# Performance work log

Hardware: AMD Instinct MI355X
Metric: run time of the kernel (lower is better)

The kernel has to match this reference:

```python
import jax, jax.numpy as jnp
import numpy as np
import math

B, T, D, H = 4, 1024, 1024, 16
DK = D // H
TAU_THRESH = 0.3


def setup_inputs() -> dict:
    key = jax.random.key(0)
    ks = jax.random.split(key, 13)
    s = 1.0 / math.sqrt(D)
    return {
        "x": jax.random.normal(ks[0], (B, T, D), dtype=jnp.float32),
        "Wq": jax.random.normal(ks[1], (D, D), dtype=jnp.float32) * s,
        "bq": jax.random.normal(ks[2], (D,), dtype=jnp.float32) * s,
        "Wk": jax.random.normal(ks[3], (D, D), dtype=jnp.float32) * s,
        "bk": jax.random.normal(ks[4], (D,), dtype=jnp.float32) * s,
        "Wv": jax.random.normal(ks[5], (D, D), dtype=jnp.float32) * s,
        "bv": jax.random.normal(ks[6], (D,), dtype=jnp.float32) * s,
        "Wo": jax.random.normal(ks[7], (D, D), dtype=jnp.float32) * s,
        "bo": jax.random.normal(ks[8], (D,), dtype=jnp.float32) * s,
        "Wg1": jax.random.normal(ks[9], (1, D), dtype=jnp.float32) * s,
        "bg1": jax.random.normal(ks[10], (1,), dtype=jnp.float32) * s,
        "Wg2": jax.random.normal(ks[11], (1, D), dtype=jnp.float32) * s,
        "bg2": jax.random.normal(ks[12], (1,), dtype=jnp.float32) * s,
    }


def reference(x, Wq, bq, Wk, bk, Wv, bv, Wo, bo, Wg1, bg1, Wg2, bg2):
    b, t, d = x.shape
    # projections (torch Linear: y = x @ W.T + b)
    Q = (x @ Wq.T + bq).reshape(b, t, H, DK).transpose(0, 2, 1, 3)  # [B,H,T,dk]
    K = (x @ Wk.T + bk).reshape(b, t, H, DK).transpose(0, 2, 1, 3)
    V = (x @ Wv.T + bv).reshape(b, t, H, DK).transpose(0, 2, 1, 3)
    scores = jnp.einsum("bhqd,bhkd->bhqk", Q, K) / math.sqrt(DK)  # [B,H,T,T]
    # confidence gates from first-token query context [B, H*dk] = [B, D]
    context = Q[:, :, 0, :].reshape(b, d)
    q1 = jax.nn.sigmoid(context @ Wg1.T + bg1)  # [B,1]
    q2 = jax.nn.sigmoid(context @ Wg2.T + bg2)  # [B,1]
    c = jnp.clip(q1 * q2, 1e-8, 1.0)            # [B,1]
    tau = jnp.where(c < TAU_THRESH, 1.0 / c, jnp.ones_like(c)).reshape(b, 1, 1, 1)
    p = jax.nn.softmax(scores / tau, axis=-1)
    cb = c.reshape(b, 1, 1, 1)
    p_gated = cb * p + (1.0 - cb) * (1.0 / t)
    u = jnp.mean(1.0 - c, axis=-1, keepdims=True)  # [B,1]
    attn_out = jnp.einsum("bhqk,bhkd->bhqd", p_gated, V)
    attn_out = attn_out.transpose(0, 2, 1, 3).reshape(b, t, d)
    output = attn_out @ Wo.T + bo
    return output, u
```

## Files before the change

### kernel.cpp

```cpp
#include <hip/hip_runtime.h>
#include <stdint.h>

typedef short bf16x8 __attribute__((ext_vector_type(8)));
typedef float f32x4 __attribute__((ext_vector_type(4)));

#define MFMA_BF16(a, b, c) __builtin_amdgcn_mfma_f32_16x16x32_bf16((a), (b), (c), 0, 0, 0)

__device__ __forceinline__ short f2bf(float x) {
  union { float f; uint32_t u; } v; v.f = x;
  uint32_t r = (v.u + 0x7FFFu + ((v.u >> 16) & 1u)) >> 16;
  return (short)r;
}
__device__ __forceinline__ uint32_t rnd_bf_hi(float x) {
  union { float f; uint32_t u; } v; v.f = x;
  return v.u + 0x7FFFu + ((v.u >> 16) & 1u);
}
__device__ __forceinline__ uint32_t pack2bf(float a, float b) {
  return __builtin_amdgcn_perm(rnd_bf_hi(b), rnd_bf_hi(a), 0x07060302);
}
__device__ __forceinline__ float bfbits2f(uint32_t b16) {
  union { uint32_t u; float f; } v; v.u = b16 << 16; return v.f;
}
__device__ __forceinline__ float fexp2(float x) {
#if __has_builtin(__builtin_amdgcn_exp2f)
  return __builtin_amdgcn_exp2f(x);
#else
  return __expf(x * 0.6931471805599453f);
#endif
}
__device__ __forceinline__ void async16(const void* g, void* l) {
  __builtin_amdgcn_global_load_lds(
      (const __attribute__((address_space(1))) uint32_t*)g,
      (__attribute__((address_space(3))) uint32_t*)l, 16, 0, 0);
}

__global__ __launch_bounds__(256) void prep_k(
    const float* __restrict__ x, const float* __restrict__ Wq,
    const float* __restrict__ Wk, const float* __restrict__ Wv,
    const float* __restrict__ Wo, const float* __restrict__ bq,
    short* __restrict__ xb, short* __restrict__ Wqb, short* __restrict__ Wkb,
    short* __restrict__ Wvb, short* __restrict__ Wob, float* __restrict__ ctx) {
  __shared__ float xs[1024];
  const int bid = blockIdx.x;
  const int tid = threadIdx.x;
  if (bid < 8192) {
    const float* src; short* dst; int idx;
    if (bid < 4096) {
      src = x; dst = xb; idx = (bid << 8) + tid;
    } else {
      const int r = bid - 4096;
      const int z = r >> 10;
      src = (z == 0) ? Wq : (z == 1) ? Wk : (z == 2) ? Wv : Wo;
      dst = (z == 0) ? Wqb : (z == 1) ? Wkb : (z == 2) ? Wvb : Wob;
      idx = ((r & 1023) << 8) + tid;
    }
    float4 v = ((const float4*)src)[idx];
    short4 o;
    o.x = f2bf(v.x); o.y = f2bf(v.y); o.z = f2bf(v.z); o.w = f2bf(v.w);
    ((short4*)dst)[idx] = o;
  } else {
    const int r = bid - 8192;
    const int b = r >> 4;
    const int n0 = (r & 15) << 6;
    for (int i = tid; i < 1024; i += 256) xs[i] = x[b * 1048576 + i];
    __syncthreads();
    const int w = tid >> 6, lane = tid & 63;
    const float4* xv4 = (const float4*)xs;
    for (int rr = 0; rr < 16; ++rr) {
      const int n = n0 + (w << 4) + rr;
      const float4* wrow = (const float4*)(Wq + n * 1024);
      float p = 0.f;
#pragma unroll
      for (int c2 = 0; c2 < 4; ++c2) {
        float4 wv = wrow[lane + (c2 << 6)];
        float4 xv = xv4[lane + (c2 << 6)];
        p += xv.x * wv.x + xv.y * wv.y + xv.z * wv.z + xv.w * wv.w;
      }
#pragma unroll
      for (int off = 32; off; off >>= 1) p += __shfl_xor(p, off);
      if (lane == 0) ctx[b * 1024 + n] = p + bq[n];
    }
  }
}

__global__ __launch_bounds__(256) void gates_fin(const float* __restrict__ ctx,
                                                 const float* __restrict__ Wg1,
                                                 const float* __restrict__ bg1,
                                                 const float* __restrict__ Wg2,
                                                 const float* __restrict__ bg2,
                                                 float* __restrict__ gates,
                                                 float* __restrict__ u_out) {
  __shared__ float red[16];
  const int tid = threadIdx.x, w = tid >> 6, lane = tid & 63;
  for (int b = 0; b < 4; ++b) {
    float4 cv = ((const float4*)(ctx + b * 1024))[tid];
    float4 w1 = ((const float4*)Wg1)[tid];
    float4 w2 = ((const float4*)Wg2)[tid];
    float p1 = cv.x * w1.x + cv.y * w1.y + cv.z * w1.z + cv.w * w1.w;
    float p2 = cv.x * w2.x + cv.y * w2.y + cv.z * w2.z + cv.w * w2.w;
#pragma unroll
    for (int off = 32; off; off >>= 1) { p1 += __shfl_xor(p1, off); p2 += __shfl_xor(p2, off); }
    if (lane == 0) { red[w] = p1; red[8 + w] = p2; }
    __syncthreads();
    if (tid == 0) {
      float g1 = red[0] + red[1] + red[2] + red[3] + bg1[0];
      float g2 = red[8] + red[9] + red[10] + red[11] + bg2[0];
      float q1 = 1.f / (1.f + expf(-g1));
      float q2 = 1.f / (1.f + expf(-g2));
      float c = fminf(fmaxf(q1 * q2, 1e-8f), 1.0f);
      gates[b * 2 + 0] = c;
      gates[b * 2 + 1] = (c < 0.3f ? c : 1.0f) * 0.125f;
      u_out[b] = 1.0f - c;
    }
    __syncthreads();
  }
}

__global__ __launch_bounds__(256) void gemm_qkv(
    const short* __restrict__ xb,
    const short* __restrict__ Wqb, const short* __restrict__ Wkb, const short* __restrict__ Wvb,
    const float* __restrict__ bq, const float* __restrict__ bk, const float* __restrict__ bv,
    const float* __restrict__ gat,
    short* __restrict__ Qh, short* __restrict__ Kh, short* __restrict__ Vt) {
  const int z = blockIdx.z;
  const short* W = (z == 0) ? Wqb : (z == 1) ? Wkb : Wvb;
  const float* bias = (z == 0) ? bq : (z == 1) ? bk : bv;

  const int m0 = blockIdx.x << 7;
  const int n0 = blockIdx.y << 7;
  const int tid = threadIdx.x;
  const int w = tid >> 6, lane = tid & 63;
  const int m15 = lane & 15, quad = lane >> 4;
  const int wr = w >> 1, wc = w & 1;

  const float qsc = (z == 0) ? gat[(m0 >> 10) * 2 + 1] * 1.4426950408889634f : 1.0f;

  __shared__ short As[4096];
  __shared__ short Bs[4096];

  f32x4 acc[4][4];
#pragma unroll
  for (int i = 0; i < 4; ++i)
#pragma unroll
    for (int j = 0; j < 4; ++j) { f32x4 zz = {0.f, 0.f, 0.f, 0.f}; acc[i][j] = zz; }

  const int s0 = tid, s1 = tid + 256;
  const int row0 = s0 >> 2, lcb0 = (s0 & 3) ^ ((row0 >> 1) & 3);
  const int row1 = s1 >> 2, lcb1 = (s1 & 3) ^ ((row1 >> 1) & 3);
  const short* ga0 = xb + (m0 + row0) * 1024 + (lcb0 << 3);
  const short* ga1 = xb + (m0 + row1) * 1024 + (lcb1 << 3);
  const short* gb0 = W + (n0 + row0) * 1024 + (lcb0 << 3);
  const short* gb1 = W + (n0 + row1) * 1024 + (lcb1 << 3);
  short* la0 = &As[s0 << 3];
  short* la1 = &As[s1 << 3];
  short* lb0 = &Bs[s0 << 3];
  short* lb1 = &Bs[s1 << 3];

  for (int kt = 0; kt < 32; ++kt) {
    async16(ga0, la0); async16(ga1, la1);
    async16(gb0, lb0); async16(gb1, lb1);
    ga0 += 32; ga1 += 32; gb0 += 32; gb1 += 32;
    __syncthreads();
    bf16x8 a[4], b[4];
#pragma unroll
    for (int i = 0; i < 4; ++i) {
      const int ra = (wr << 6) + (i << 4) + m15;
      a[i] = *(const bf16x8*)(&As[ra * 32 + ((quad ^ ((ra >> 1) & 3)) << 3)]);
    }
#pragma unroll
    for (int j = 0; j < 4; ++j) {
      const int rb = (wc << 6) + (j << 4) + m15;
      b[j] = *(const bf16x8*)(&Bs[rb * 32 + ((quad ^ ((rb >> 1) & 3)) << 3)]);
    }
#pragma unroll
    for (int i = 0; i < 4; ++i)
#pragma unroll
      for (int j = 0; j < 4; ++j)
        acc[i][j] = MFMA_BF16(a[i], b[j], acc[i][j]);
    __syncthreads();
  }

  if (z == 2) {
    const int batch = m0 >> 10;
#pragma unroll
    for (int j = 0; j < 4; ++j) {
      const int n = n0 + (wc << 6) + (j << 4) + m15;
      const float bb_ = bias[n];
      const int h = n >> 6, dk = n & 63;
      short* vrow = Vt + ((((batch << 4) + h) << 6) + dk) * 1024;
#pragma unroll
      for (int i = 0; i < 4; ++i) {
        const int t = (m0 & 1023) + (wr << 6) + (i << 4) + (quad << 2);
        uint2 pk;
        pk.x = pack2bf(acc[i][j][0] + bb_, acc[i][j][1] + bb_);
        pk.y = pack2bf(acc[i][j][2] + bb_, acc[i][j][3] + bb_);
        *(uint2*)(vrow + t) = pk;
      }
    }
  } else {
#pragma unroll
    for (int j = 0; j < 4; ++j) {
      const int n = n0 + (wc << 6) + (j << 4) + m15;
      const float bb_ = bias[n];
      const int h = n >> 6, dk = n & 63;
#pragma unroll
      for (int i = 0; i < 4; ++i) {
        const int mb = m0 + (wr << 6) + (i << 4) + (quad << 2);
#pragma unroll
        for (int r = 0; r < 4; ++r) {
          const int m = mb + r;
          const int batch = m >> 10, t = m & 1023;
          const short o = f2bf((acc[i][j][r] + bb_) * qsc);
          if (z == 1) Kh[((batch * 16 + h) * 1024 + t) * 64 + dk] = o;
          else        Qh[((batch * 16 + h) * 1024 + t) * 64 + dk] = o;
        }
      }
    }
  }
}

__global__ __launch_bounds__(256) void gemm_out(const short* __restrict__ Ab,
                                                const short* __restrict__ Wo,
                                                const float* __restrict__ bo,
                                                float* __restrict__ Cout) {
  const int m0 = blockIdx.x << 6;
  const int n0 = blockIdx.y << 7;
  const int tid = threadIdx.x;
  const int w = tid >> 6, lane = tid & 63;
  const int m15 = lane & 15, quad = lane >> 4;
  const int wr = w >> 1, wc = w & 1;

  __shared__ short As[2048];
  __shared__ short Bs[4096];

  f32x4 acc[2][4];
#pragma unroll
  for (int i = 0; i < 2; ++i)
#pragma unroll
    for (int j = 0; j < 4; ++j) { f32x4 zz = {0.f, 0.f, 0.f, 0.f}; acc[i][j] = zz; }

  const int s0 = tid, s1 = tid + 256;
  const int arow = s0 >> 2, alcb = (s0 & 3) ^ ((arow >> 1) & 3);
  const int brow0 = s0 >> 2, blcb0 = alcb;
  const int brow1 = s1 >> 2, blcb1 = (s1 & 3) ^ ((brow1 >> 1) & 3);
  const short* gA  = Ab + (m0 + arow) * 1024 + (alcb << 3);
  const short* gB0 = Wo + (n0 + brow0) * 1024 + (blcb0 << 3);
  const short* gB1 = Wo + (n0 + brow1) * 1024 + (blcb1 << 3);
  short* lA  = &As[s0 << 3];
  short* lB0 = &Bs[s0 << 3];
  short* lB1 = &Bs[s1 << 3];

  for (int kt = 0; kt < 32; ++kt) {
    async16(gA, lA);
    async16(gB0, lB0); async16(gB1, lB1);
    gA += 32; gB0 += 32; gB1 += 32;
    __syncthreads();
    bf16x8 a[2], b[4];
#pragma unroll
    for (int i = 0; i < 2; ++i) {
      const int ra = (wr << 5) + (i << 4) + m15;
      a[i] = *(const bf16x8*)(&As[ra * 32 + ((quad ^ ((ra >> 1) & 3)) << 3)]);
    }
#pragma unroll
    for (int j = 0; j < 4; ++j) {
      const int rb = (wc << 6) + (j << 4) + m15;
      b[j] = *(const bf16x8*)(&Bs[rb * 32 + ((quad ^ ((rb >> 1) & 3)) << 3)]);
    }
#pragma unroll
    for (int i = 0; i < 2; ++i)
#pragma unroll
      for (int j = 0; j < 4; ++j)
        acc[i][j] = MFMA_BF16(a[i], b[j], acc[i][j]);
    __syncthreads();
  }

#pragma unroll
  for (int j = 0; j < 4; ++j) {
    const int n = n0 + (wc << 6) + (j << 4) + m15;
    const float bb_ = bo[n];
#pragma unroll
    for (int i = 0; i < 2; ++i) {
      const int mb = m0 + (wr << 5) + (i << 4) + (quad << 2);
#pragma unroll
      for (int r = 0; r < 4; ++r)
        Cout[(mb + r) * 1024 + n] = acc[i][j][r] + bb_;
    }
  }
}

__global__ __launch_bounds__(256) void meanv_k(const short* __restrict__ Vt,
                                               float* __restrict__ meanV) {
  const int bh = blockIdx.x;
  const int tid = threadIdx.x;
  const int d = tid >> 2, part = tid & 3;
  const short* row = Vt + bh * 65536 + d * 1024 + part * 256;
  float s = 0.f;
#pragma unroll 4
  for (int i = 0; i < 64; ++i) {
    uint2 v = *(const uint2*)(row + i * 4);
    s += bfbits2f(v.x & 0xffffu) + bfbits2f(v.x >> 16) +
         bfbits2f(v.y & 0xffffu) + bfbits2f(v.y >> 16);
  }
  s += __shfl_xor(s, 1);
  s += __shfl_xor(s, 2);
  if (part == 0) meanV[bh * 64 + d] = s * (1.0f / 1024.0f);
}

__global__ __launch_bounds__(256, 4) void attn_k(const short* __restrict__ Qh,
                                                 const short* __restrict__ Kh,
                                                 const short* __restrict__ Vt,
                                                 const float* __restrict__ gates,
                                                 const float* __restrict__ meanV,
                                                 short* __restrict__ attnb) {
  const int bh = blockIdx.x;
  const int b = bh >> 4, h = bh & 15;
  const int q0 = blockIdx.y << 6;
  const int tid = threadIdx.x;
  const int w = tid >> 6, lane = tid & 63;
  const int m15 = lane & 15, quad = lane >> 4;

  __shared__ short Ks[2][4096];
  __shared__ short Vs[2][4096];

  const short* ksrc = Kh + bh * 65536;
  const short* vsrc = Vt + bh * 65536;

  const short* qsrc = Qh + ((bh << 10) + q0 + (w << 4) + m15) * 64;
  const bf16x8 qb0 = *(const bf16x8*)(qsrc + (quad << 3));
  const bf16x8 qb1 = *(const bf16x8*)(qsrc + 32 + (quad << 3));

  const int off0 = tid, off1 = tid + 256;
  const int r0 = off0 >> 3, cb0 = (off0 & 7) ^ (r0 & 7);
  const int r1 = off1 >> 3, cb1 = (off1 & 7) ^ (r1 & 7);

#define STAGE(kv, bufi)                                                        \
  do {                                                                         \
    async16(ksrc + (((kv) << 6) + r0) * 64 + (cb0 << 3), &Ks[bufi][off0 << 3]);\
    async16(ksrc + (((kv) << 6) + r1) * 64 + (cb1 << 3), &Ks[bufi][off1 << 3]);\
    async16(vsrc + r0 * 1024 + ((kv) << 6) + (cb0 << 3), &Vs[bufi][off0 << 3]);\
    async16(vsrc + r1 * 1024 + ((kv) << 6) + (cb1 << 3), &Vs[bufi][off1 << 3]);\
  } while (0)

  STAGE(0, 0);

  float lsum = 0.f;
  f32x4 o_acc[4];
#pragma unroll
  for (int jd = 0; jd < 4; ++jd) { f32x4 zz = {0.f, 0.f, 0.f, 0.f}; o_acc[jd] = zz; }

  const int srcA = ((quad & 1) << 5) + m15;
  const int srcB = srcA + 16;
  const bool selhi = (quad & 2) != 0;

  for (int kv = 0; kv < 16; ++kv) {
    __syncthreads();
    if (kv < 15) STAGE(kv + 1, (kv + 1) & 1);
    const short* Kb = &Ks[kv & 1][0];
    const short* Vb = &Vs[kv & 1][0];

    f32x4 sacc[4];
#pragma unroll
    for (int s = 0; s < 4; ++s) {
      const int row = (s << 4) + m15;
      const int sw = row & 7;
      bf16x8 a0 = *(const bf16x8*)(Kb + (row << 6) + ((quad ^ sw) << 3));
      bf16x8 a1 = *(const bf16x8*)(Kb + (row << 6) + (((quad + 4) ^ sw) << 3));
      f32x4 zz = {0.f, 0.f, 0.f, 0.f};
      zz = MFMA_BF16(a0, qb0, zz);
      zz = MFMA_BF16(a1, qb1, zz);
      sacc[s] = zz;
    }

    uint32_t pk[4][2];
#pragma unroll
    for (int s = 0; s < 4; ++s) {
      float p0 = fexp2(sacc[s][0]);
      float p1 = fexp2(sacc[s][1]);
      float p2 = fexp2(sacc[s][2]);
      float p3 = fexp2(sacc[s][3]);
      lsum += (p0 + p1) + (p2 + p3);
      pk[s][0] = pack2bf(p0, p1);
      pk[s][1] = pack2bf(p2, p3);
    }

    bf16x8 pf[2];
#pragma unroll
    for (int H = 0; H < 2; ++H) {
      uint32_t f[4];
#pragma unroll
      for (int rp = 0; rp < 2; ++rp) {
        uint32_t alo = (uint32_t)__shfl((int)pk[2 * H][rp], srcA);
        uint32_t ahi = (uint32_t)__shfl((int)pk[2 * H + 1][rp], srcA);
        uint32_t blo = (uint32_t)__shfl((int)pk[2 * H][rp], srcB);
        uint32_t bhi = (uint32_t)__shfl((int)pk[2 * H + 1][rp], srcB);
        f[rp]     = selhi ? ahi : alo;
        f[2 + rp] = selhi ? bhi : blo;
      }
      pf[H] = *(bf16x8*)f;
    }

#pragma unroll
    for (int jd = 0; jd < 4; ++jd) {
      const int row = (jd << 4) + m15;
      const int sw = row & 7;
      bf16x8 v0 = *(const bf16x8*)(Vb + (row << 6) + ((quad ^ sw) << 3));
      bf16x8 v1 = *(const bf16x8*)(Vb + (row << 6) + (((quad + 4) ^ sw) << 3));
      o_acc[jd] = MFMA_BF16(v0, pf[0], o_acc[jd]);
      o_acc[jd] = MFMA_BF16(v1, pf[1], o_acc[jd]);
    }
  }
#undef STAGE

  float l = lsum;
  l += __shfl_xor(l, 16);
  l += __shfl_xor(l, 32);

  const float cg = gates[b * 2 + 0];
  const float s0 = cg / l;
  const float omc = 1.0f - cg;
  const int qrow = q0 + (w << 4) + m15;
  short* orow = attnb + ((b << 10) + qrow) * 1024 + (h << 6);
#pragma unroll
  for (int jd = 0; jd < 4; ++jd) {
    float4 mv = *(const float4*)(meanV + (bh << 6) + (jd << 4) + (quad << 2));
    float v0_ = s0 * o_acc[jd][0] + omc * mv.x;
    float v1_ = s0 * o_acc[jd][1] + omc * mv.y;
    float v2_ = s0 * o_acc[jd][2] + omc * mv.z;
    float v3_ = s0 * o_acc[jd][3] + omc * mv.w;
    uint2 st;
    st.x = pack2bf(v0_, v1_);
    st.y = pack2bf(v2_, v3_);
    *(uint2*)(orow + (jd << 4) + (quad << 2)) = st;
  }
}

extern "C" void kernel_launch(void* const* d_in, const int* in_sizes, int n_in,
                              void* d_out, int out_size, void* d_ws, size_t ws_size,
                              hipStream_t stream) {
  const float* x   = (const float*)d_in[0];
  const float* Wq  = (const float*)d_in[1];
  const float* bq  = (const float*)d_in[2];
  const float* Wk  = (const float*)d_in[3];
  const float* bk  = (const float*)d_in[4];
  const float* Wv  = (const float*)d_in[5];
  const float* bv  = (const float*)d_in[6];
  const float* Wo  = (const float*)d_in[7];
  const float* bo  = (const float*)d_in[8];
  const float* Wg1 = (const float*)d_in[9];
  const float* bg1 = (const float*)d_in[10];
  const float* Wg2 = (const float*)d_in[11];
  const float* bg2 = (const float*)d_in[12];
  float* out = (float*)d_out;

  char* ws = (char*)d_ws;
  short* xb   = (short*)(ws + 0);
  short* Wqb  = (short*)(ws + 8388608);
  short* Wkb  = (short*)(ws + 10485760);
  short* Wvb  = (short*)(ws + 12582912);
  short* Wob  = (short*)(ws + 14680064);
  short* Qh   = (short*)(ws + 16777216);
  short* Kh   = (short*)(ws + 25165824);
  short* Vt   = (short*)(ws + 33554432);
  short* attb = (short*)(ws + 41943040);
  float* ctx  = (float*)(ws + 50331648);
  float* gat  = (float*)(ws + 50348032);
  float* mV   = (float*)(ws + 50348064);

  prep_k<<<8256, 256, 0, stream>>>(x, Wq, Wk, Wv, Wo, bq,
                                   xb, Wqb, Wkb, Wvb, Wob, ctx);
  gates_fin<<<1, 256, 0, stream>>>(ctx, Wg1, bg1, Wg2, bg2, gat, out + 4194304);

  gemm_qkv<<<dim3(32, 8, 3), 256, 0, stream>>>(xb, Wqb, Wkb, Wvb, bq, bk, bv, gat, Qh, Kh, Vt);
  meanv_k<<<64, 256, 0, stream>>>(Vt, mV);
  attn_k<<<dim3(64, 16), 256, 0, stream>>>(Qh, Kh, Vt, gat, mV, attb);
  gemm_out<<<dim3(64, 8), 256, 0, stream>>>(attb, Wob, bo, out);
}
```

Measured before the change: 218.6 us.

## Move softmax scale into attention, drop LDS swizzle and packed Vt stores

The temperature/log2e scale moves from Q at projection time into the attention exp (multiply per score). The QKV GEMM drops the XOR LDS swizzle in favour of a plain row layout, and replaces the packed 8-byte transposed V stores with per-element scalar stores. The mean-of-V division by 1024 moves into the attention epilogue coefficient. These changes add a per-score multiply, likely LDS bank conflicts, and uncoalesced V writes, so they read more like a simplification than a speedup.

```diff
diff --git a/kernel.cpp b/kernel.cpp
--- a/kernel.cpp
+++ b/kernel.cpp
@@ -109,7 +109,7 @@
       float q2 = 1.f / (1.f + expf(-g2));
       float c = fminf(fmaxf(q1 * q2, 1e-8f), 1.0f);
       gates[b * 2 + 0] = c;
-      gates[b * 2 + 1] = (c < 0.3f ? c : 1.0f) * 0.125f;
+      gates[b * 2 + 1] = (c < 0.3f ? c : 1.0f) * 0.125f * 1.4426950408889634f;
       u_out[b] = 1.0f - c;
     }
     __syncthreads();
@@ -120,7 +120,6 @@
     const short* __restrict__ xb,
     const short* __restrict__ Wqb, const short* __restrict__ Wkb, const short* __restrict__ Wvb,
     const float* __restrict__ bq, const float* __restrict__ bk, const float* __restrict__ bv,
-    const float* __restrict__ gat,
     short* __restrict__ Qh, short* __restrict__ Kh, short* __restrict__ Vt) {
   const int z = blockIdx.z;
   const short* W = (z == 0) ? Wqb : (z == 1) ? Wkb : Wvb;
@@ -133,8 +132,6 @@
   const int m15 = lane & 15, quad = lane >> 4;
   const int wr = w >> 1, wc = w & 1;
 
-  const float qsc = (z == 0) ? gat[(m0 >> 10) * 2 + 1] * 1.4426950408889634f : 1.0f;
-
   __shared__ short As[4096];
   __shared__ short Bs[4096];
 
@@ -144,17 +141,16 @@
 #pragma unroll
     for (int j = 0; j < 4; ++j) { f32x4 zz = {0.f, 0.f, 0.f, 0.f}; acc[i][j] = zz; }
 
-  const int s0 = tid, s1 = tid + 256;
-  const int row0 = s0 >> 2, lcb0 = (s0 & 3) ^ ((row0 >> 1) & 3);
-  const int row1 = s1 >> 2, lcb1 = (s1 & 3) ^ ((row1 >> 1) & 3);
-  const short* ga0 = xb + (m0 + row0) * 1024 + (lcb0 << 3);
-  const short* ga1 = xb + (m0 + row1) * 1024 + (lcb1 << 3);
-  const short* gb0 = W + (n0 + row0) * 1024 + (lcb0 << 3);
-  const short* gb1 = W + (n0 + row1) * 1024 + (lcb1 << 3);
-  short* la0 = &As[s0 << 3];
-  short* la1 = &As[s1 << 3];
-  short* lb0 = &Bs[s0 << 3];
-  short* lb1 = &Bs[s1 << 3];
+  const int srow = (w << 5) + (lane >> 2);
+  const int scol = (lane & 3) << 3;
+  const short* ga0 = xb + (m0 + srow) * 1024 + scol;
+  const short* ga1 = ga0 + 16 * 1024;
+  const short* gb0 = W + (n0 + srow) * 1024 + scol;
+  const short* gb1 = gb0 + 16 * 1024;
+  short* la0 = &As[srow * 32 + scol];
+  short* la1 = la0 + 512;
+  short* lb0 = &Bs[srow * 32 + scol];
+  short* lb1 = lb0 + 512;
 
   for (int kt = 0; kt < 32; ++kt) {
     async16(ga0, la0); async16(ga1, la1);
@@ -163,15 +159,11 @@
     __syncthreads();
     bf16x8 a[4], b[4];
 #pragma unroll
-    for (int i = 0; i < 4; ++i) {
-      const int ra = (wr << 6) + (i << 4) + m15;
-      a[i] = *(const bf16x8*)(&As[ra * 32 + ((quad ^ ((ra >> 1) & 3)) << 3)]);
-    }
-#pragma unroll
-    for (int j = 0; j < 4; ++j) {
-      const int rb = (wc << 6) + (j << 4) + m15;
-      b[j] = *(const bf16x8*)(&Bs[rb * 32 + ((quad ^ ((rb >> 1) & 3)) << 3)]);
-    }
+    for (int i = 0; i < 4; ++i)
+      a[i] = *(const bf16x8*)(&As[((wr << 6) + (i << 4) + m15) * 32 + (quad << 3)]);
+#pragma unroll
+    for (int j = 0; j < 4; ++j)
+      b[j] = *(const bf16x8*)(&Bs[((wc << 6) + (j << 4) + m15) * 32 + (quad << 3)]);
 #pragma unroll
     for (int i = 0; i < 4; ++i)
 #pragma unroll
@@ -180,39 +172,25 @@
     __syncthreads();
   }
 
-  if (z == 2) {
-    const int batch = m0 >> 10;
-#pragma unroll
-    for (int j = 0; j < 4; ++j) {
-      const int n = n0 + (wc << 6) + (j << 4) + m15;
-      const float bb_ = bias[n];
-      const int h = n >> 6, dk = n & 63;
-      short* vrow = Vt + ((((batch << 4) + h) << 6) + dk) * 1024;
-#pragma unroll
-      for (int i = 0; i < 4; ++i) {
-        const int t = (m0 & 1023) + (wr << 6) + (i << 4) + (quad << 2);
-        uint2 pk;
-        pk.x = pack2bf(acc[i][j][0] + bb_, acc[i][j][1] + bb_);
-        pk.y = pack2bf(acc[i][j][2] + bb_, acc[i][j][3] + bb_);
-        *(uint2*)(vrow + t) = pk;
-      }
-    }
-  } else {
-#pragma unroll
-    for (int j = 0; j < 4; ++j) {
-      const int n = n0 + (wc << 6) + (j << 4) + m15;
-      const float bb_ = bias[n];
-      const int h = n >> 6, dk = n & 63;
-#pragma unroll
-      for (int i = 0; i < 4; ++i) {
-        const int mb = m0 + (wr << 6) + (i << 4) + (quad << 2);
-#pragma unroll
-        for (int r = 0; r < 4; ++r) {
-          const int m = mb + r;
-          const int batch = m >> 10, t = m & 1023;
-          const short o = f2bf((acc[i][j][r] + bb_) * qsc);
-          if (z == 1) Kh[((batch * 16 + h) * 1024 + t) * 64 + dk] = o;
-          else        Qh[((batch * 16 + h) * 1024 + t) * 64 + dk] = o;
+#pragma unroll
+  for (int j = 0; j < 4; ++j) {
+    const int n = n0 + (wc << 6) + (j << 4) + m15;
+    const float bb_ = bias[n];
+    const int h = n >> 6, dk = n & 63;
+#pragma unroll
+    for (int i = 0; i < 4; ++i) {
+      const int mb = m0 + (wr << 6) + (i << 4) + (quad << 2);
+#pragma unroll
+      for (int r = 0; r < 4; ++r) {
+        const int m = mb + r;
+        const int batch = m >> 10, t = m & 1023;
+        const short o = f2bf(acc[i][j][r] + bb_);
+        if (z == 2) {
+          Vt[((batch * 16 + h) * 64 + dk) * 1024 + t] = o;
+        } else if (z == 1) {
+          Kh[((batch * 16 + h) * 1024 + t) * 64 + dk] = o;
+        } else {
+          Qh[((batch * 16 + h) * 1024 + t) * 64 + dk] = o;
         }
       }
     }
@@ -241,10 +219,9 @@
 
   const int s0 = tid, s1 = tid + 256;
   const int arow = s0 >> 2, alcb = (s0 & 3) ^ ((arow >> 1) & 3);
-  const int brow0 = s0 >> 2, blcb0 = alcb;
   const int brow1 = s1 >> 2, blcb1 = (s1 & 3) ^ ((brow1 >> 1) & 3);
   const short* gA  = Ab + (m0 + arow) * 1024 + (alcb << 3);
-  const short* gB0 = Wo + (n0 + brow0) * 1024 + (blcb0 << 3);
+  const short* gB0 = Wo + (n0 + arow) * 1024 + (alcb << 3);
   const short* gB1 = Wo + (n0 + brow1) * 1024 + (blcb1 << 3);
   short* lA  = &As[s0 << 3];
   short* lB0 = &Bs[s0 << 3];
@@ -289,7 +266,7 @@
 }
 
 __global__ __launch_bounds__(256) void meanv_k(const short* __restrict__ Vt,
-                                               float* __restrict__ meanV) {
+                                               float* __restrict__ mV) {
   const int bh = blockIdx.x;
   const int tid = threadIdx.x;
   const int d = tid >> 2, part = tid & 3;
@@ -303,14 +280,14 @@
   }
   s += __shfl_xor(s, 1);
   s += __shfl_xor(s, 2);
-  if (part == 0) meanV[bh * 64 + d] = s * (1.0f / 1024.0f);
+  if (part == 0) mV[bh * 64 + d] = s;
 }
 
 __global__ __launch_bounds__(256, 4) void attn_k(const short* __restrict__ Qh,
                                                  const short* __restrict__ Kh,
                                                  const short* __restrict__ Vt,
                                                  const float* __restrict__ gates,
-                                                 const float* __restrict__ meanV,
+                                                 const float* __restrict__ mV,
                                                  short* __restrict__ attnb) {
   const int bh = blockIdx.x;
   const int b = bh >> 4, h = bh & 15;
@@ -324,6 +301,8 @@
 
   const short* ksrc = Kh + bh * 65536;
   const short* vsrc = Vt + bh * 65536;
+
+  const float sl = gates[b * 2 + 1];
 
   const short* qsrc = Qh + ((bh << 10) + q0 + (w << 4) + m15) * 64;
   const bf16x8 qb0 = *(const bf16x8*)(qsrc + (quad << 3));
@@ -374,10 +353,10 @@
     uint32_t pk[4][2];
 #pragma unroll
     for (int s = 0; s < 4; ++s) {
-      float p0 = fexp2(sacc[s][0]);
-      float p1 = fexp2(sacc[s][1]);
-      float p2 = fexp2(sacc[s][2]);
-      float p3 = fexp2(sacc[s][3]);
+      float p0 = fexp2(sacc[s][0] * sl);
+      float p1 = fexp2(sacc[s][1] * sl);
+      float p2 = fexp2(sacc[s][2] * sl);
+      float p3 = fexp2(sacc[s][3] * sl);
       lsum += (p0 + p1) + (p2 + p3);
       pk[s][0] = pack2bf(p0, p1);
       pk[s][1] = pack2bf(p2, p3);
@@ -417,16 +396,16 @@
 
   const float cg = gates[b * 2 + 0];
   const float s0 = cg / l;
-  const float omc = 1.0f - cg;
+  const float coef = (1.0f - cg) * (1.0f / 1024.0f);
   const int qrow = q0 + (w << 4) + m15;
   short* orow = attnb + ((b << 10) + qrow) * 1024 + (h << 6);
 #pragma unroll
   for (int jd = 0; jd < 4; ++jd) {
-    float4 mv = *(const float4*)(meanV + (bh << 6) + (jd << 4) + (quad << 2));
-    float v0_ = s0 * o_acc[jd][0] + omc * mv.x;
-    float v1_ = s0 * o_acc[jd][1] + omc * mv.y;
-    float v2_ = s0 * o_acc[jd][2] + omc * mv.z;
-    float v3_ = s0 * o_acc[jd][3] + omc * mv.w;
+    float4 mv = *(const float4*)(mV + (bh << 6) + (jd << 4) + (quad << 2));
+    float v0_ = s0 * o_acc[jd][0] + coef * mv.x;
+    float v1_ = s0 * o_acc[jd][1] + coef * mv.y;
+    float v2_ = s0 * o_acc[jd][2] + coef * mv.z;
+    float v3_ = s0 * o_acc[jd][3] + coef * mv.w;
     uint2 st;
     st.x = pack2bf(v0_, v1_);
     st.y = pack2bf(v2_, v3_);
@@ -470,7 +449,8 @@
                                    xb, Wqb, Wkb, Wvb, Wob, ctx);
   gates_fin<<<1, 256, 0, stream>>>(ctx, Wg1, bg1, Wg2, bg2, gat, out + 4194304);
 
-  gemm_qkv<<<dim3(32, 8, 3), 256, 0, stream>>>(xb, Wqb, Wkb, Wvb, bq, bk, bv, gat, Qh, Kh, Vt);
+  gemm_qkv<<<dim3(32, 8, 3), 256, 0, stream>>>(xb, Wqb, Wkb, Wvb, bq, bk, bv,
+                                               Qh, Kh, Vt);
   meanv_k<<<64, 256, 0, stream>>>(Vt, mV);
   attn_k<<<dim3(64, 16), 256, 0, stream>>>(Qh, Kh, Vt, gat, mV, attb);
   gemm_out<<<dim3(64, 8), 256, 0, stream>>>(attb, Wob, bo, out);
```

Result: faster. 212.5 us (median of 2 runs) (-2.8%).
